# Optimization experiments

Hardware: AMD Instinct MI355X
Metric: run time of the kernel (lower is better)

Reference implementation:

```python
import jax, jax.numpy as jnp
import numpy as np

B, HQ, HKV, D, S = 32, 32, 8, 128, 4096
POOL = B * S
SCALING = 0.08838834764831845  # 1/sqrt(128)
LOGIT_CAP = 0.0                # disabled


def setup_inputs() -> dict:
    key = jax.random.key(0)
    ks = jax.random.split(key, 5)
    q = jax.random.normal(ks[0], (B, HQ, D), dtype=jnp.float32)
    k = jax.random.normal(ks[1], (B, HKV, D), dtype=jnp.float32)
    v = jax.random.normal(ks[2], (B, HKV, D), dtype=jnp.float32)
    k_pool = jax.random.normal(ks[3], (POOL, HKV, D), dtype=jnp.float32)
    v_pool = jax.random.normal(ks[4], (POOL, HKV, D), dtype=jnp.float32)
    # contiguous page layout: request b owns slots [b*S, (b+1)*S)
    kv_indices = jnp.arange(B * S, dtype=jnp.int32).reshape(B, S)
    # new token of each request is written to its last slot
    out_cache_loc = kv_indices[:, -1]
    return {"q": q, "k": k, "v": v, "k_pool": k_pool, "v_pool": v_pool,
            "kv_indices": kv_indices, "out_cache_loc": out_cache_loc}


def reference(q, k, v, k_pool, v_pool, kv_indices, out_cache_loc):
    # 1) save_kv_cache: write new k/v into the paged pool
    k_pool = k_pool.at[out_cache_loc].set(k)
    v_pool = v_pool.at[out_cache_loc].set(v)
    # 2) gather each request's KV pages: [B, S, HKV, D]
    K = k_pool[kv_indices]
    V = v_pool[kv_indices]
    # 3) grouped-query attention (HQ = HKV * G)
    G = HQ // HKV
    qg = q.reshape(B, HKV, G, D)
    scores = jnp.einsum('bhgd,bshd->bhgs', qg, K) * SCALING
    if LOGIT_CAP > 0.0:
        scores = LOGIT_CAP * jnp.tanh(scores / LOGIT_CAP)
    p = jax.nn.softmax(scores, axis=-1)
    out = jnp.einsum('bhgs,bshd->bhgd', p, V).reshape(B, HQ, D)
    return out
```

## Files before the change

### kernel.cpp

```cpp
#include <hip/hip_runtime.h>
#include <math.h>

#define BB   32
#define HQn  32
#define HKVn 8
#define Dn   128
#define Sn   4096
#define Gn   4
#define NWAVES 16
#define TPH  (Sn / (NWAVES * 2))
#define SCALING 0.08838834764831845f

__global__ void scatter_kv(const float* __restrict__ k, const float* __restrict__ v,
                           const int* __restrict__ loc,
                           float* __restrict__ kp, float* __restrict__ vp) {
    int t  = blockIdx.x * blockDim.x + threadIdx.x;
    int b  = t >> 10;
    int hd = t & 1023;
    int p  = loc[b];
    size_t dst = (size_t)p * (HKVn * Dn) + hd;
    kp[dst] = k[t];
    vp[dst] = v[t];
}

__launch_bounds__(1024, 1)
__global__ void attn_decode(const float* __restrict__ q,
                            const float* __restrict__ k_pool,
                            const float* __restrict__ v_pool,
                            const int*   __restrict__ kv_indices,
                            float* __restrict__ out) {
    const int bh   = blockIdx.x;
    const int b    = bh >> 3;
    const int hkv  = bh & 7;
    const int tid  = threadIdx.x;
    const int wave = tid >> 6;
    const int lane = tid & 63;
    const int half = lane >> 5;
    const int c    = lane & 31;
    const int part = wave * 2 + half;

    __shared__ float s_out[NWAVES][Gn][Dn];
    __shared__ float s_m[NWAVES][Gn];
    __shared__ float s_l[NWAVES][Gn];

    float4 qf[Gn];
#pragma unroll
    for (int g = 0; g < Gn; g++) {
        const float4* q4 = (const float4*)(q + ((size_t)b * HQn + hkv * Gn + g) * Dn);
        float4 t = q4[c];
        qf[g] = make_float4(t.x * SCALING, t.y * SCALING, t.z * SCALING, t.w * SCALING);
    }

    const int*    idxrow = kv_indices + (size_t)b * Sn;
    const float4* kp4 = (const float4*)k_pool;
    const float4* vp4 = (const float4*)v_pool;
    const int rowstride = HKVn * Dn / 4;
    const int hoff      = hkv * (Dn / 4);

    float  m[Gn], l[Gn];
    float4 acc[Gn];
#pragma unroll
    for (int g = 0; g < Gn; g++) {
        m[g] = -INFINITY; l[g] = 0.f;
        acc[g] = make_float4(0.f, 0.f, 0.f, 0.f);
    }

    int    idx0 = idxrow[part];
    float4 kf = kp4[(size_t)idx0 * rowstride + hoff + c];
    float4 vf = vp4[(size_t)idx0 * rowstride + hoff + c];

    for (int i = 0; i < TPH; i++) {
        int sn = i * 32 + part + 32;
        if (sn >= Sn) sn -= Sn;
        int idxn = idxrow[sn];
        float4 kn = kp4[(size_t)idxn * rowstride + hoff + c];
        float4 vn = vp4[(size_t)idxn * rowstride + hoff + c];

#pragma unroll
        for (int g = 0; g < Gn; g++) {
            float dot = qf[g].x * kf.x + qf[g].y * kf.y + qf[g].z * kf.z + qf[g].w * kf.w;
            dot += __shfl_xor(dot, 1, 64);
            dot += __shfl_xor(dot, 2, 64);
            dot += __shfl_xor(dot, 4, 64);
            dot += __shfl_xor(dot, 8, 64);
            dot += __shfl_xor(dot, 16, 64);
            float mn    = fmaxf(m[g], dot);
            float scale = __expf(m[g] - mn);
            float w     = __expf(dot - mn);
            m[g] = mn;
            l[g] = l[g] * scale + w;
            acc[g].x = acc[g].x * scale + w * vf.x;
            acc[g].y = acc[g].y * scale + w * vf.y;
            acc[g].z = acc[g].z * scale + w * vf.z;
            acc[g].w = acc[g].w * scale + w * vf.w;
        }
        kf = kn; vf = vn;
    }

#pragma unroll
    for (int g = 0; g < Gn; g++) {
        float mo = __shfl_xor(m[g], 32, 64);
        float lo = __shfl_xor(l[g], 32, 64);
        float4 ao;
        ao.x = __shfl_xor(acc[g].x, 32, 64);
        ao.y = __shfl_xor(acc[g].y, 32, 64);
        ao.z = __shfl_xor(acc[g].z, 32, 64);
        ao.w = __shfl_xor(acc[g].w, 32, 64);
        float M  = fmaxf(m[g], mo);
        float w1 = __expf(m[g] - M);
        float w2 = __expf(mo   - M);
        m[g] = M;
        l[g] = l[g] * w1 + lo * w2;
        acc[g].x = acc[g].x * w1 + ao.x * w2;
        acc[g].y = acc[g].y * w1 + ao.y * w2;
        acc[g].z = acc[g].z * w1 + ao.z * w2;
        acc[g].w = acc[g].w * w1 + ao.w * w2;
    }

    if (half == 0) {
#pragma unroll
        for (int g = 0; g < Gn; g++) {
            ((float4*)&s_out[wave][g][0])[c] = acc[g];
            if (c == 0) { s_m[wave][g] = m[g]; s_l[wave][g] = l[g]; }
        }
    }
    __syncthreads();

    if (tid < Gn * Dn) {
        int g = tid >> 7;
        int d = tid & 127;
        float M = -INFINITY;
#pragma unroll
        for (int p = 0; p < NWAVES; p++) M = fmaxf(M, s_m[p][g]);
        float L = 0.f, O = 0.f;
#pragma unroll
        for (int p = 0; p < NWAVES; p++) {
            float w = __expf(s_m[p][g] - M);
            L += w * s_l[p][g];
            O += w * s_out[p][g][d];
        }
        out[((size_t)b * HQn + hkv * Gn + g) * Dn + d] = O / L;
    }
}

extern "C" void kernel_launch(void* const* d_in, const int* in_sizes, int n_in,
                              void* d_out, int out_size, void* d_ws, size_t ws_size,
                              hipStream_t stream) {
    const float* q       = (const float*)d_in[0];
    const float* k       = (const float*)d_in[1];
    const float* v       = (const float*)d_in[2];
    float* k_pool        = (float*)d_in[3];
    float* v_pool        = (float*)d_in[4];
    const int* kv_indices    = (const int*)d_in[5];
    const int* out_cache_loc = (const int*)d_in[6];
    float* out = (float*)d_out;

    scatter_kv<<<(BB * HKVn * Dn) / 256, 256, 0, stream>>>(k, v, out_cache_loc, k_pool, v_pool);
    attn_decode<<<BB * HKVn, 1024, 0, stream>>>(q, k_pool, v_pool, kv_indices, out);
}
```

Baseline: 971.7 us.

## Process two tokens per half-wave, preload indices via shuffles, use nontemporal loads

Each half-wave now handles two tokens per iteration, which halves the loop trip count and doubles the K/V loads in flight. The two tokens share one online-softmax rescale. Each half-wave preloads its kv_indices into registers and broadcasts them with shuffles, removing a dependent global index load from every iteration. K/V loads become nontemporal so they skip cache retention, and vector-extension types shorten the arithmetic. Register pressure goes up and token ordering changes, but the math is equivalent.

```diff
diff --git a/kernel.cpp b/kernel.cpp
--- a/kernel.cpp
+++ b/kernel.cpp
@@ -8,8 +8,11 @@
 #define Sn   4096
 #define Gn   4
 #define NWAVES 16
-#define TPH  (Sn / (NWAVES * 2))
+#define NHW   (NWAVES * 2)
+#define TOKITER (Sn / (NHW * 2))
 #define SCALING 0.08838834764831845f
+
+typedef float f32x4 __attribute__((ext_vector_type(4)));
 
 __global__ void scatter_kv(const float* __restrict__ k, const float* __restrict__ v,
                            const int* __restrict__ loc,
@@ -43,65 +46,78 @@
     __shared__ float s_m[NWAVES][Gn];
     __shared__ float s_l[NWAVES][Gn];
 
-    float4 qf[Gn];
+    f32x4 qf[Gn];
 #pragma unroll
     for (int g = 0; g < Gn; g++) {
-        const float4* q4 = (const float4*)(q + ((size_t)b * HQn + hkv * Gn + g) * Dn);
-        float4 t = q4[c];
-        qf[g] = make_float4(t.x * SCALING, t.y * SCALING, t.z * SCALING, t.w * SCALING);
+        const f32x4* q4 = (const f32x4*)(q + ((size_t)b * HQn + hkv * Gn + g) * Dn);
+        qf[g] = q4[c] * SCALING;
     }
 
-    const int*    idxrow = kv_indices + (size_t)b * Sn;
-    const float4* kp4 = (const float4*)k_pool;
-    const float4* vp4 = (const float4*)v_pool;
+    const int* idxrow = kv_indices + (size_t)b * Sn;
+    int ireg[4];
+#pragma unroll
+    for (int r = 0; r < 4; r++) {
+        int i = (r & 1) * 32 + c;
+        int j = r >> 1;
+        ireg[r] = idxrow[i * 64 + part * 2 + j];
+    }
+
+    const f32x4* kp4 = (const f32x4*)k_pool;
+    const f32x4* vp4 = (const f32x4*)v_pool;
     const int rowstride = HKVn * Dn / 4;
-    const int hoff      = hkv * (Dn / 4);
+    const int hoff      = hkv * (Dn / 4) + c;
 
-    float  m[Gn], l[Gn];
-    float4 acc[Gn];
+    float m[Gn], l[Gn];
+    f32x4 acc[Gn];
 #pragma unroll
     for (int g = 0; g < Gn; g++) {
         m[g] = -INFINITY; l[g] = 0.f;
-        acc[g] = make_float4(0.f, 0.f, 0.f, 0.f);
+        acc[g] = (f32x4)(0.f);
     }
 
-    int    idx0 = idxrow[part];
-    float4 kf = kp4[(size_t)idx0 * rowstride + hoff + c];
-    float4 vf = vp4[(size_t)idx0 * rowstride + hoff + c];
+    int idx0 = __shfl(ireg[0], 0, 32);
+    int idx1 = __shfl(ireg[2], 0, 32);
+    f32x4 kf0 = __builtin_nontemporal_load(kp4 + (size_t)idx0 * rowstride + hoff);
+    f32x4 vf0 = __builtin_nontemporal_load(vp4 + (size_t)idx0 * rowstride + hoff);
+    f32x4 kf1 = __builtin_nontemporal_load(kp4 + (size_t)idx1 * rowstride + hoff);
+    f32x4 vf1 = __builtin_nontemporal_load(vp4 + (size_t)idx1 * rowstride + hoff);
 
-    for (int i = 0; i < TPH; i++) {
-        int sn = i * 32 + part + 32;
-        if (sn >= Sn) sn -= Sn;
-        int idxn = idxrow[sn];
-        float4 kn = kp4[(size_t)idxn * rowstride + hoff + c];
-        float4 vn = vp4[(size_t)idxn * rowstride + hoff + c];
+    for (int i = 0; i < TOKITER; i++) {
+        int inext = (i < TOKITER - 1) ? i + 1 : i;
+        int rb  = inext >> 5;
+        int src = inext & 31;
+        int nidx0 = __shfl(ireg[rb],     src, 32);
+        int nidx1 = __shfl(ireg[2 + rb], src, 32);
+        f32x4 kn0 = __builtin_nontemporal_load(kp4 + (size_t)nidx0 * rowstride + hoff);
+        f32x4 vn0 = __builtin_nontemporal_load(vp4 + (size_t)nidx0 * rowstride + hoff);
+        f32x4 kn1 = __builtin_nontemporal_load(kp4 + (size_t)nidx1 * rowstride + hoff);
+        f32x4 vn1 = __builtin_nontemporal_load(vp4 + (size_t)nidx1 * rowstride + hoff);
 
 #pragma unroll
         for (int g = 0; g < Gn; g++) {
-            float dot = qf[g].x * kf.x + qf[g].y * kf.y + qf[g].z * kf.z + qf[g].w * kf.w;
-            dot += __shfl_xor(dot, 1, 64);
-            dot += __shfl_xor(dot, 2, 64);
-            dot += __shfl_xor(dot, 4, 64);
-            dot += __shfl_xor(dot, 8, 64);
-            dot += __shfl_xor(dot, 16, 64);
-            float mn    = fmaxf(m[g], dot);
-            float scale = __expf(m[g] - mn);
-            float w     = __expf(dot - mn);
+            float d0 = qf[g].x * kf0.x + qf[g].y * kf0.y + qf[g].z * kf0.z + qf[g].w * kf0.w;
+            float d1 = qf[g].x * kf1.x + qf[g].y * kf1.y + qf[g].z * kf1.z + qf[g].w * kf1.w;
+            d0 += __shfl_xor(d0, 1, 64);  d1 += __shfl_xor(d1, 1, 64);
+            d0 += __shfl_xor(d0, 2, 64);  d1 += __shfl_xor(d1, 2, 64);
+            d0 += __shfl_xor(d0, 4, 64);  d1 += __shfl_xor(d1, 4, 64);
+            d0 += __shfl_xor(d0, 8, 64);  d1 += __shfl_xor(d1, 8, 64);
+            d0 += __shfl_xor(d0, 16, 64); d1 += __shfl_xor(d1, 16, 64);
+            float mn = fmaxf(m[g], fmaxf(d0, d1));
+            float sc = __expf(m[g] - mn);
+            float w0 = __expf(d0 - mn);
+            float w1 = __expf(d1 - mn);
             m[g] = mn;
-            l[g] = l[g] * scale + w;
-            acc[g].x = acc[g].x * scale + w * vf.x;
-            acc[g].y = acc[g].y * scale + w * vf.y;
-            acc[g].z = acc[g].z * scale + w * vf.z;
-            acc[g].w = acc[g].w * scale + w * vf.w;
+            l[g] = l[g] * sc + w0 + w1;
+            acc[g] = acc[g] * sc + vf0 * w0 + vf1 * w1;
         }
-        kf = kn; vf = vn;
+        kf0 = kn0; vf0 = vn0; kf1 = kn1; vf1 = vn1;
     }
 
 #pragma unroll
     for (int g = 0; g < Gn; g++) {
         float mo = __shfl_xor(m[g], 32, 64);
         float lo = __shfl_xor(l[g], 32, 64);
-        float4 ao;
+        f32x4 ao;
         ao.x = __shfl_xor(acc[g].x, 32, 64);
         ao.y = __shfl_xor(acc[g].y, 32, 64);
         ao.z = __shfl_xor(acc[g].z, 32, 64);
@@ -111,16 +127,13 @@
         float w2 = __expf(mo   - M);
         m[g] = M;
         l[g] = l[g] * w1 + lo * w2;
-        acc[g].x = acc[g].x * w1 + ao.x * w2;
-        acc[g].y = acc[g].y * w1 + ao.y * w2;
-        acc[g].z = acc[g].z * w1 + ao.z * w2;
-        acc[g].w = acc[g].w * w1 + ao.w * w2;
+        acc[g] = acc[g] * w1 + ao * w2;
     }
 
     if (half == 0) {
 #pragma unroll
         for (int g = 0; g < Gn; g++) {
-            ((float4*)&s_out[wave][g][0])[c] = acc[g];
+            ((f32x4*)&s_out[wave][g][0])[c] = acc[g];
             if (c == 0) { s_m[wave][g] = m[g]; s_l[wave][g] = l[g]; }
         }
     }
```

After: 930.6 us. 4.2% less time.
